# Kernel tuning notes

Hardware: AMD Instinct MI355X
Metric: run time of the kernel (lower is better)

Reference implementation:

```python
import jax, jax.numpy as jnp
import numpy as np

B, S, E, H, D, NE, R = 2, 2048, 2048, 16, 128, 8, 16
HALF = D // 2
THETA = 10000.0


def setup_inputs() -> dict:
    key = jax.random.key(0)
    ks = jax.random.split(key, 18)

    def w(k, shape, fan_in):
        return jax.random.normal(k, shape, jnp.float32) / np.float32(np.sqrt(fan_in))

    inp = {
        "x": jax.random.normal(ks[0], (B, S, E), jnp.float32),
        "expert_mask": jax.random.uniform(ks[1], (B, S, NE), dtype=jnp.float32),
    }
    for i, n in enumerate(("q", "k", "v")):
        inp["W" + n] = w(ks[2 + 3 * i], (H * D, E), E)
        inp["b" + n] = jnp.zeros((H * D,), jnp.float32)
        inp["A" + n] = w(ks[3 + 3 * i], (NE, R, E), E)
        inp["B" + n] = w(ks[4 + 3 * i], (H * D, NE, R), R)
    inp["Wo"] = w(ks[11], (E, H * D), H * D)
    inp["bo"] = jnp.zeros((E,), jnp.float32)
    inp["Ao"] = w(ks[12], (NE, R, H * D), H * D)
    inp["Bo"] = w(ks[13], (E, NE, R), R)
    return inp


def routed_linear(x, W, b, A, Bm, mask):
    """MaybeRoutedLinear: dense base + expert-routed low-rank path gated by mask [B,S,NE]."""
    y = jnp.einsum("bsi,oi->bso", x, W) + b
    h = jnp.einsum("bsi,eri->bser", x, A) * mask[..., None]  # [B,S,NE,R]
    return y + jnp.einsum("bser,oer->bso", h, Bm)


def apply_rope(t):
    """Llama-style rotary embedding. t: [B,S,H,D]."""
    inv_freq = 1.0 / (THETA ** (jnp.arange(0, D, 2, dtype=jnp.float32) / D))  # [D/2]
    freqs = jnp.arange(S, dtype=jnp.float32)[:, None] * inv_freq[None, :]  # [S,D/2]
    cos = jnp.concatenate([jnp.cos(freqs)] * 2, -1)[None, :, None, :]  # [1,S,1,D]
    sin = jnp.concatenate([jnp.sin(freqs)] * 2, -1)[None, :, None, :]
    rot = jnp.concatenate([-t[..., HALF:], t[..., :HALF]], -1)
    return t * cos + rot * sin


def reference(x, expert_mask, Wq, bq, Aq, Bq, Wk, bk, Ak, Bk, Wv, bv, Av, Bv, Wo, bo, Ao, Bo):
    q = routed_linear(x, Wq, bq, Aq, Bq, expert_mask).reshape(B, S, H, D)
    k = routed_linear(x, Wk, bk, Ak, Bk, expert_mask).reshape(B, S, H, D)
    v = routed_linear(x, Wv, bv, Av, Bv, expert_mask).reshape(B, S, H, D)
    q = apply_rope(q)
    k = apply_rope(k)
    scores = jnp.einsum("bqhd,bkhd->bhqk", q, k) / jnp.float32(np.sqrt(D))
    causal = jnp.tril(jnp.ones((S, S), dtype=bool))
    scores = jnp.where(causal[None, None], scores, jnp.finfo(scores.dtype).min)
    probs = jax.nn.softmax(scores, axis=-1)
    o = jnp.einsum("bhqk,bkhd->bqhd", probs, v).reshape(B, S, H * D)
    return routed_linear(o, Wo, bo, Ao, Bo, expert_mask)
```

## Files before the change

kernel.cpp:

```cpp
#include <hip/hip_runtime.h>


#define B_ 2
#define S_ 2048
#define E_ 2048
#define H_ 16
#define D_ 128
#define NE_ 8
#define R_ 16
#define HD_ 2048
#define M_ 4096
#define KL_ 128

typedef unsigned short u16;
typedef unsigned int u32;
typedef __attribute__((ext_vector_type(8))) short bf16x8;
typedef __attribute__((ext_vector_type(4))) float f32x4;

typedef const __attribute__((address_space(1))) void gvoid_t;
typedef __attribute__((address_space(3))) void svoid_t;

__device__ __forceinline__ float bf2f(u16 u) {
    union { u32 i; float f; } v; v.i = ((u32)u) << 16; return v.f;
}
__device__ __forceinline__ u16 f2bf(float f) {
    union { float f; u32 i; } v; v.f = f;
    u32 x = v.i;
    return (u16)((x + 0x7fffu + ((x >> 16) & 1u)) >> 16);
}
__device__ __forceinline__ float ldf(const void* p, size_t i, int f) {
    return f ? ((const float*)p)[i] : bf2f(((const u16*)p)[i]);
}
__device__ __forceinline__ float4 ld4(const void* p, size_t i, int f) {
    if (f) return *(const float4*)((const float*)p + i);
    ushort4 v = *(const ushort4*)((const u16*)p + i);
    return make_float4(bf2f(v.x), bf2f(v.y), bf2f(v.z), bf2f(v.w));
}

__global__ void k_detect(const void* __restrict__ x, int* __restrict__ flags) {
    __shared__ int votes[2];
    int tid = threadIdx.x;
    if (tid < 2) votes[tid] = 0;
    __syncthreads();
    const u32* p = (const u32*)x;
    int bad = 0, tot = 0;
    for (int i = tid; i < 4096; i += 64) {
        u32 lo = p[i] & 0xffffu;
        if (lo) {
            tot++;
            int e = (int)((lo >> 7) & 0xffu);
            if (e < 100 || e > 150) bad++;
        }
    }
    atomicAdd(&votes[0], bad);
    atomicAdd(&votes[1], tot);
    __syncthreads();
    if (tid == 0) flags[0] = (votes[1] > 0 && votes[0] * 10 > votes[1] * 3) ? 1 : 0;
}

__global__ void k_cvt(const void* __restrict__ src, u16* __restrict__ dst, int n,
                      const int* __restrict__ flags) {
    int fin = flags[0];
    int i = (blockIdx.x * 256 + threadIdx.x) * 4;
    if (i >= n) return;
    float4 v = ld4(src, i, fin);
    ushort4 o;
    o.x = f2bf(v.x); o.y = f2bf(v.y); o.z = f2bf(v.z); o.w = f2bf(v.w);
    *(ushort4*)(dst + i) = o;
}

__global__ void k_cvtf(const float* __restrict__ src, u16* __restrict__ dst, int n) {
    int i = (blockIdx.x * 256 + threadIdx.x) * 4;
    if (i >= n) return;
    float4 v = *(const float4*)(src + i);
    ushort4 o;
    o.x = f2bf(v.x); o.y = f2bf(v.y); o.z = f2bf(v.z); o.w = f2bf(v.w);
    *(ushort4*)(dst + i) = o;
}

__global__ void k_zero(float4* __restrict__ p, int n4) {
    int i = blockIdx.x * 256 + threadIdx.x;
    if (i < n4) p[i] = make_float4(0.f, 0.f, 0.f, 0.f);
}

#define NX_  8388608L
#define NA1_ 262144L
#define NW_  4194304L
__global__ void k_cvt_all(
    const void* __restrict__ x,
    const void* __restrict__ Aq, const void* __restrict__ Ak,
    const void* __restrict__ Av, const void* __restrict__ Ao,
    const void* __restrict__ Bq, const void* __restrict__ Bk,
    const void* __restrict__ Bv, const void* __restrict__ Bo,
    const void* __restrict__ Wq, const void* __restrict__ Wk,
    const void* __restrict__ Wv,
    u16* __restrict__ Xb, u16* __restrict__ Acat, u16* __restrict__ Bmcat,
    u16* __restrict__ Wcat,
    const int* __restrict__ flags) {
    int fin = flags[0];
    long i = (long)(blockIdx.x * 256 + threadIdx.x) * 4;
    const void* src; u16* dst; long off;
    if (i < NX_) { src = x; dst = Xb; off = i; }
    else if (i < NX_ + 4 * NA1_) {
        long j = i - NX_; int p = (int)(j >> 18); off = j & (NA1_ - 1);
        src = (p == 0) ? Aq : (p == 1) ? Ak : (p == 2) ? Av : Ao;
        dst = Acat + (long)p * NA1_;
    } else if (i < NX_ + 8 * NA1_) {
        long j = i - NX_ - 4 * NA1_; int p = (int)(j >> 18); off = j & (NA1_ - 1);
        src = (p == 0) ? Bq : (p == 1) ? Bk : (p == 2) ? Bv : Bo;
        dst = Bmcat + (long)p * NA1_;
    } else {
        long j = i - NX_ - 8 * NA1_; int p = (int)(j / NW_); off = j - (long)p * NW_;
        src = (p == 0) ? Wq : (p == 1) ? Wk : Wv;
        dst = Wcat + (long)p * NW_;
    }
    float4 v = ld4(src, off, fin);
    ushort4 o;
    o.x = f2bf(v.x); o.y = f2bf(v.y); o.z = f2bf(v.z); o.w = f2bf(v.w);
    *(ushort4*)(dst + off) = o;
}

#define BM_ 128
#define BN_ 128
#define BK_ 64

__global__ __launch_bounds__(256, 2) void k_gemm_sk(
    const u16* __restrict__ A, int lda,
    const u16* __restrict__ Bw, int ldb, int K,
    const void* __restrict__ mask,
    float* __restrict__ Cf, int ldc,
    const int* __restrict__ flags) {
    __shared__ __align__(16) u16 As[BM_ * BK_];
    __shared__ __align__(16) u16 Bs[BN_ * BK_];
    int fin = flags[0];
    int tid = threadIdx.x;
    int w = tid >> 6, lane = tid & 63;
    int l15 = lane & 15, quad = lane >> 4;
    int wm = w >> 1, wn = w & 1;
    int m0 = blockIdx.y * BM_, n0 = blockIdx.x * BN_;
    int lrow = lane >> 3;
    int lcol = (lane & 7) * 8;

    f32x4 acc[4][4];
#pragma unroll
    for (int mt = 0; mt < 4; mt++)
#pragma unroll
        for (int nt = 0; nt < 4; nt++)
#pragma unroll
            for (int r = 0; r < 4; r++) acc[mt][nt][r] = 0.f;

    int iters = (K / BK_) / gridDim.z;
    int it0 = blockIdx.z * iters;
    for (int it = it0; it < it0 + iters; it++) {
        int kb = it * BK_;
        __syncthreads();
#pragma unroll
        for (int i = 0; i < 4; i++) {
            int rowb = (w * 4 + i) * 8;
            int r = rowb + lrow;
            __builtin_amdgcn_global_load_lds(
                (gvoid_t*)(A + (size_t)(m0 + r) * lda + kb + lcol),
                (svoid_t*)(As + rowb * BK_), 16, 0, 0);
            __builtin_amdgcn_global_load_lds(
                (gvoid_t*)(Bw + (size_t)(n0 + r) * ldb + kb + lcol),
                (svoid_t*)(Bs + rowb * BK_), 16, 0, 0);
        }
        __syncthreads();
#pragma unroll
        for (int kk = 0; kk < 2; kk++) {
            int ko = kk * 32 + quad * 8;
            bf16x8 af[4], bf[4];
#pragma unroll
            for (int mt = 0; mt < 4; mt++)
                af[mt] = *(const bf16x8*)(As + (wm * 64 + mt * 16 + l15) * BK_ + ko);
#pragma unroll
            for (int nt = 0; nt < 4; nt++)
                bf[nt] = *(const bf16x8*)(Bs + (wn * 64 + nt * 16 + l15) * BK_ + ko);
#pragma unroll
            for (int mt = 0; mt < 4; mt++)
#pragma unroll
                for (int nt = 0; nt < 4; nt++)
                    acc[mt][nt] = __builtin_amdgcn_mfma_f32_16x16x32_bf16(
                        af[mt], bf[nt], acc[mt][nt], 0, 0, 0);
        }
    }

#pragma unroll
    for (int mt = 0; mt < 4; mt++) {
#pragma unroll
        for (int r = 0; r < 4; r++) {
            int m = m0 + wm * 64 + mt * 16 + quad * 4 + r;
#pragma unroll
            for (int nt = 0; nt < 4; nt++) {
                int n = n0 + wn * 64 + nt * 16 + l15;
                float v = acc[mt][nt][r] * ldf(mask, (size_t)m * NE_ + ((n & 127) >> 4), fin);
                atomicAdd(&Cf[(size_t)m * ldc + n], v);
            }
        }
    }
}

template <int BNt>
__global__ __launch_bounds__(512, 2) void k_gemm256(
    const u16* __restrict__ A, int lda,
    const u16* __restrict__ Bw, int ldb, int K1,
    const u16* __restrict__ A2, int lda2,
    const u16* __restrict__ B2, int K2,
    const void* __restrict__ bias0, const void* __restrict__ bias1,
    const void* __restrict__ bias2,
    void* __restrict__ C, int ldc, int store_mode,
    const int* __restrict__ flags) {
    constexpr int NTF = BNt / 64;
    __shared__ __align__(16) u16 As[2][256 * 32];
    __shared__ __align__(16) u16 Bs[2][BNt * 32];
    int fin = flags[0];
    int tid = threadIdx.x;
    int w = tid >> 6, lane = tid & 63;
    int l15 = lane & 15, quad = lane >> 4;
    int wm = w >> 2, wn = w & 3;

    int lin = blockIdx.y * gridDim.x + blockIdx.x;
    int cpx = (gridDim.x * gridDim.y) >> 3;
    int wg = (lin & 7) * cpx + (lin >> 3);
    int m0 = (wg / gridDim.x) * 256;
    int n0 = (wg % gridDim.x) * BNt;

    int p = (store_mode == 3) ? (n0 >> 11) : 0;
    const u16* A2p = A2 + p * 128;
    const u16* B2p = B2 + (long)p * NA1_;
    int nloc = (store_mode == 3) ? (n0 & 2047) : n0;

    int nk1 = K1 >> 5;
    int NT = nk1 + (K2 >> 5);

    f32x4 acc[8][NTF];
#pragma unroll
    for (int mt = 0; mt < 8; mt++)
#pragma unroll
        for (int nt = 0; nt < NTF; nt++)
#pragma unroll
            for (int r = 0; r < 4; r++) acc[mt][nt][r] = 0.f;

    auto stage = [&](int kt) {
        const u16 *pa, *pb; size_t sa, sb; int kb, nb;
        if (kt < nk1) { pa = A;   sa = lda;  pb = Bw;  sb = ldb; kb = kt * 32; nb = n0; }
        else          { pa = A2p; sa = lda2; pb = B2p; sb = K2;  kb = (kt - nk1) * 32; nb = nloc; }
        int buf = kt & 1;
#pragma unroll
        for (int j = 0; j < 2; j++) {
            int s = w * 2 + j;
            __builtin_amdgcn_global_load_lds(
                (gvoid_t*)(pa + (size_t)(m0 + s * 16 + l15) * sa + kb + quad * 8),
                (svoid_t*)(&As[buf][s * 512]), 16, 0, 0);
        }
        if constexpr (BNt == 256) {
#pragma unroll
            for (int j = 0; j < 2; j++) {
                int s = w * 2 + j;
                __builtin_amdgcn_global_load_lds(
                    (gvoid_t*)(pb + (size_t)(nb + s * 16 + l15) * sb + kb + quad * 8),
                    (svoid_t*)(&Bs[buf][s * 512]), 16, 0, 0);
            }
        } else {
            __builtin_amdgcn_global_load_lds(
                (gvoid_t*)(pb + (size_t)(nb + w * 16 + l15) * sb + kb + quad * 8),
                (svoid_t*)(&Bs[buf][w * 512]), 16, 0, 0);
        }
    };

    stage(0);
    for (int kt = 0; kt < NT; kt++) {
        int buf = kt & 1;
        if (kt + 1 < NT) {
            stage(kt + 1);
            if constexpr (BNt == 256) asm volatile("s_waitcnt vmcnt(4)" ::: "memory");
            else                      asm volatile("s_waitcnt vmcnt(3)" ::: "memory");
        } else {
            asm volatile("s_waitcnt vmcnt(0)" ::: "memory");
        }
        __builtin_amdgcn_s_barrier();
        __builtin_amdgcn_sched_barrier(0);

        bf16x8 af[8], bfr[NTF];
#pragma unroll
        for (int mt = 0; mt < 8; mt++)
            af[mt] = *(const bf16x8*)(&As[buf][(wm * 8 + mt) * 512 + lane * 8]);
#pragma unroll
        for (int nt = 0; nt < NTF; nt++)
            bfr[nt] = *(const bf16x8*)(&Bs[buf][(wn * NTF + nt) * 512 + lane * 8]);

        __builtin_amdgcn_s_setprio(1);
#pragma unroll
        for (int mt = 0; mt < 8; mt++)
#pragma unroll
            for (int nt = 0; nt < NTF; nt++)
                acc[mt][nt] = __builtin_amdgcn_mfma_f32_16x16x32_bf16(
                    af[mt], bfr[nt], acc[mt][nt], 0, 0, 0);
        __builtin_amdgcn_s_setprio(0);

        __builtin_amdgcn_s_barrier();
        __builtin_amdgcn_sched_barrier(0);
    }

    const void* bp = (store_mode == 3) ? (p == 0 ? bias0 : p == 1 ? bias1 : bias2)
                                       : bias0;
#pragma unroll
    for (int mt = 0; mt < 8; mt++) {
#pragma unroll
        for (int r = 0; r < 4; r++) {
            int m = m0 + wm * 128 + mt * 16 + quad * 4 + r;
#pragma unroll
            for (int nt = 0; nt < NTF; nt++) {
                int n = n0 + wn * (BNt / 4) + nt * 16 + l15;
                float v = acc[mt][nt][r];
                if (bp) v += ldf(bp, (size_t)(n & 2047), fin);
                if (store_mode == 3) {
                    ((u16*)C)[(size_t)p * 8388608 + (size_t)m * 2048 + (n & 2047)] = f2bf(v);
                } else {
                    if (fin) ((float*)C)[(size_t)m * ldc + n] = v;
                    else     ((u16*)C)[(size_t)m * ldc + n] = f2bf(v);
                }
            }
        }
    }
}

__global__ void k_rope2(u16* __restrict__ Q, u16* __restrict__ K) {
    const int n = M_ * HD_ / 2;
    int idx = blockIdx.x * 256 + threadIdx.x;
    u16* Y = (idx < n) ? Q : K;
    int id = (idx < n) ? idx : idx - n;
    int d2 = id & 63;
    int sh = id >> 6;
    int s = (sh >> 4) & (S_ - 1);
    float inv = powf(10000.f, -(float)d2 * (1.f / 64.f));
    float fr = (float)s * inv;
    float c, sn;
    sincosf(fr, &sn, &c);
    size_t base = ((size_t)sh) << 7;
    float t0 = bf2f(Y[base + d2]);
    float t1 = bf2f(Y[base + d2 + 64]);
    Y[base + d2]      = f2bf(t0 * c - t1 * sn);
    Y[base + d2 + 64] = f2bf(t1 * c + t0 * sn);
}

__global__ void k_transpose_v(const u16* __restrict__ Vb, u16* __restrict__ Vt) {
    __shared__ u16 t[32][33];
    int s0 = blockIdx.x * 32;
    int n0 = blockIdx.y * 32;
    int b  = blockIdx.z;
    int tx = threadIdx.x & 31, ty = threadIdx.x >> 5;
#pragma unroll
    for (int r = 0; r < 4; r++)
        t[ty + r * 8][tx] = Vb[((size_t)(b * S_ + s0 + ty + r * 8)) * HD_ + n0 + tx];
    __syncthreads();
#pragma unroll
    for (int r = 0; r < 4; r++)
        Vt[((size_t)(b * HD_ + n0 + ty + r * 8)) * S_ + s0 + tx] = t[tx][ty + r * 8];
}

#define KS_ST 136
#define VT_ST 72
#define SCALE_ 0.088388347648318447f

__global__ __launch_bounds__(256, 3) void k_flash6(
    const u16* __restrict__ Q, const u16* __restrict__ K,
    const u16* __restrict__ Vt, u16* __restrict__ O) {
    __shared__ __align__(16) u16 Ks[64 * KS_ST];
    __shared__ __align__(16) u16 Vs[128 * VT_ST];
    __shared__ __align__(16) u16 Ps[64 * VT_ST];
    int tid = threadIdx.x;
    int w = tid >> 6, lane = tid & 63;
    int l15 = lane & 15, quad = lane >> 4;
    int bh = blockIdx.y, b = bh >> 4, h = bh & 15;
    int t = 31 - blockIdx.x;
    int q0 = t * 64;

    int krow[4], kd8[4], vd[4], vkg[4];
#pragma unroll
    for (int it = 0; it < 4; it++) {
        int idx = it * 256 + tid;
        krow[it] = idx >> 4; kd8[it] = (idx & 15) * 8;
        vd[it] = idx >> 3;   vkg[it] = (idx & 7) * 8;
    }

    bf16x8 qf[4];
    size_t baseQ = ((size_t)(b * S_ + q0 + w * 16 + l15)) * HD_ + h * D_;
#pragma unroll
    for (int ks = 0; ks < 4; ks++)
        qf[ks] = *(const bf16x8*)(Q + baseQ + ks * 32 + quad * 8);

    f32x4 of[8];
#pragma unroll
    for (int nt = 0; nt < 8; nt++)
#pragma unroll
        for (int r = 0; r < 4; r++) of[nt][r] = 0.f;
    float mreg = -30000.f, lreg = 0.f;
    int qrow = q0 + w * 16 + l15;

    int nch = t + 1;

    bf16x8 kpre[4], vpre[4];
#pragma unroll
    for (int it = 0; it < 4; it++) {
        kpre[it] = *(const bf16x8*)(K + ((size_t)(b * S_ + krow[it])) * HD_ + h * D_ + kd8[it]);
        vpre[it] = *(const bf16x8*)(Vt + ((size_t)(bh * 128 + vd[it])) * S_ + vkg[it]);
    }

    for (int c = 0; c < nch; c++) {
        int k0 = c * 64;
        __syncthreads();
#pragma unroll
        for (int it = 0; it < 4; it++) {
            *(bf16x8*)(Ks + krow[it] * KS_ST + kd8[it]) = kpre[it];
            *(bf16x8*)(Vs + vd[it] * VT_ST + vkg[it]) = vpre[it];
        }
        __syncthreads();
        if (c + 1 < nch) {
            int k1 = k0 + 64;
#pragma unroll
            for (int it = 0; it < 4; it++) {
                kpre[it] = *(const bf16x8*)(K + ((size_t)(b * S_ + k1 + krow[it])) * HD_ + h * D_ + kd8[it]);
                vpre[it] = *(const bf16x8*)(Vt + ((size_t)(bh * 128 + vd[it])) * S_ + k1 + vkg[it]);
            }
        }

        f32x4 sf[4];
#pragma unroll
        for (int nt = 0; nt < 4; nt++)
#pragma unroll
            for (int r = 0; r < 4; r++) sf[nt][r] = 0.f;
#pragma unroll
        for (int ks = 0; ks < 4; ks++) {
            int koff = ks * 32 + quad * 8;
            bf16x8 qa = qf[ks];
#pragma unroll
            for (int nt = 0; nt < 4; nt++) {
                bf16x8 kb = *(const bf16x8*)(Ks + (nt * 16 + l15) * KS_ST + koff);
                sf[nt] = __builtin_amdgcn_mfma_f32_16x16x32_bf16(kb, qa, sf[nt], 0, 0, 0);
            }
        }

#pragma unroll
        for (int nt = 0; nt < 4; nt++) {
            int keyb = k0 + nt * 16 + quad * 4;
#pragma unroll
            for (int r = 0; r < 4; r++) {
                float sv = sf[nt][r] * SCALE_;
                sf[nt][r] = (keyb + r > qrow) ? -30000.f : sv;
            }
        }

        float t0 = fmaxf(fmaxf(sf[0][0], sf[0][1]), fmaxf(sf[0][2], sf[0][3]));
        float t1 = fmaxf(fmaxf(sf[1][0], sf[1][1]), fmaxf(sf[1][2], sf[1][3]));
        float t2 = fmaxf(fmaxf(sf[2][0], sf[2][1]), fmaxf(sf[2][2], sf[2][3]));
        float t3 = fmaxf(fmaxf(sf[3][0], sf[3][1]), fmaxf(sf[3][2], sf[3][3]));
        float cmax = fmaxf(fmaxf(t0, t1), fmaxf(t2, t3));
        cmax = fmaxf(cmax, __shfl_xor(cmax, 16, 64));
        cmax = fmaxf(cmax, __shfl_xor(cmax, 32, 64));
        float mnew = fmaxf(mreg, cmax);
        float a = __expf(mreg - mnew);
        mreg = mnew;
#pragma unroll
        for (int nt = 0; nt < 4; nt++)
#pragma unroll
            for (int r = 0; r < 4; r++)
                sf[nt][r] = __expf(sf[nt][r] - mnew);
        float s0 = (sf[0][0] + sf[0][1]) + (sf[0][2] + sf[0][3]);
        float s1 = (sf[1][0] + sf[1][1]) + (sf[1][2] + sf[1][3]);
        float s2 = (sf[2][0] + sf[2][1]) + (sf[2][2] + sf[2][3]);
        float s3 = (sf[3][0] + sf[3][1]) + (sf[3][2] + sf[3][3]);
        float psum = (s0 + s1) + (s2 + s3);
        psum += __shfl_xor(psum, 16, 64);
        psum += __shfl_xor(psum, 32, 64);
        lreg = lreg * a + psum;

        float al[4];
#pragma unroll
        for (int r = 0; r < 4; r++) al[r] = __shfl(a, quad * 4 + r, 16);

#pragma unroll
        for (int nt = 0; nt < 4; nt++)
#pragma unroll
            for (int r = 0; r < 4; r++)
                Ps[(w * 16 + l15) * VT_ST + nt * 16 + quad * 4 + r] = f2bf(sf[nt][r]);
#pragma unroll
        for (int nt = 0; nt < 8; nt++)
#pragma unroll
            for (int r = 0; r < 4; r++) of[nt][r] *= al[r];

#pragma unroll
        for (int ks2 = 0; ks2 < 2; ks2++) {
            int koff = ks2 * 32 + quad * 8;
            bf16x8 pa = *(const bf16x8*)(Ps + (w * 16 + l15) * VT_ST + koff);
#pragma unroll
            for (int nt = 0; nt < 8; nt++) {
                bf16x8 vb = *(const bf16x8*)(Vs + (nt * 16 + l15) * VT_ST + koff);
                of[nt] = __builtin_amdgcn_mfma_f32_16x16x32_bf16(pa, vb, of[nt], 0, 0, 0);
            }
        }
    }

    float linv = 1.f / lreg;
    float inv[4];
#pragma unroll
    for (int r = 0; r < 4; r++) inv[r] = __shfl(linv, quad * 4 + r, 16);
    int rowb = q0 + w * 16 + quad * 4;
#pragma unroll
    for (int r = 0; r < 4; r++) {
        size_t base = ((size_t)(b * S_ + rowb + r)) * HD_ + h * D_;
#pragma unroll
        for (int nt = 0; nt < 8; nt++)
            O[base + nt * 16 + l15] = f2bf(of[nt][r] * inv[r]);
    }
}

extern "C" void kernel_launch(void* const* d_in, const int* in_sizes, int n_in,
                              void* d_out, int out_size, void* d_ws, size_t ws_size,
                              hipStream_t stream) {
    const void* x    = d_in[0];
    const void* mask = d_in[1];
    const void* Wq = d_in[2];  const void* bq = d_in[3];
    const void* Aq = d_in[4];  const void* Bq = d_in[5];
    const void* Wk = d_in[6];  const void* bk = d_in[7];
    const void* Ak = d_in[8];  const void* Bk = d_in[9];
    const void* Wv = d_in[10]; const void* bv = d_in[11];
    const void* Av = d_in[12]; const void* Bv = d_in[13];
    const void* Wo = d_in[14]; const void* bo = d_in[15];
    const void* Ao = d_in[16]; const void* Bo = d_in[17];

    char* ws = (char*)d_ws;
    const long MB = 1 << 20;
    int* flags = (int*)ws;
    u16* Xb    = (u16*)(ws + 1  * MB);
    u16* Acat  = (u16*)(ws + 17 * MB);
    u16* Bmcat = (u16*)(ws + 19 * MB);
    u16* hg3   = (u16*)(ws + 21 * MB);
    u16* hgo   = (u16*)(ws + 24 * MB);
    u16* Qb    = (u16*)(ws + 25 * MB);
    u16* Kb    = (u16*)(ws + 41 * MB);
    u16* Vb    = (u16*)(ws + 57 * MB);
    u16* Vt    = (u16*)(ws + 73 * MB);
    u16* Wcat  = (u16*)(ws + 73 * MB);
    float* hg3f = (float*)Qb;
    float* hgof = (float*)Kb;
    u16* Wob   = Qb;
    u16* Ob    = Vb;

    k_detect<<<1, 64, 0, stream>>>(x, flags);
    k_zero<<<1536, 256, 0, stream>>>((float4*)hg3f, 393216);
    const long NCVT = NX_ + 8 * NA1_ + 3 * NW_;
    k_cvt_all<<<NCVT / 1024, 256, 0, stream>>>(
        x, Aq, Ak, Av, Ao, Bq, Bk, Bv, Bo, Wq, Wk, Wv,
        Xb, Acat, Bmcat, Wcat, flags);

    k_gemm_sk<<<dim3(3, M_ / BM_, 4), 256, 0, stream>>>(
        Xb, E_, Acat, E_, E_, mask, hg3f, 384, flags);
    k_cvtf<<<1536, 256, 0, stream>>>(hg3f, hg3, 1572864);

    k_gemm256<256><<<dim3(6144 / 256, M_ / 256), 512, 0, stream>>>(
        Xb, E_, Wcat, E_, E_, hg3, 384, Bmcat, KL_,
        bq, bk, bv, Qb, HD_, 3, flags);

    k_rope2<<<(M_ * HD_) / 256, 256, 0, stream>>>(Qb, Kb);
    k_transpose_v<<<dim3(S_ / 32, HD_ / 32, B_), 256, 0, stream>>>(Vb, Vt);

    k_flash6<<<dim3(32, 32), 256, 0, stream>>>(Qb, Kb, Vt, Ob);

    k_zero<<<512, 256, 0, stream>>>((float4*)hgof, 131072);
    k_cvt<<<NW_ / 1024, 256, 0, stream>>>(Wo, Wob, (int)NW_, flags);
    k_gemm_sk<<<dim3(1, M_ / BM_, 4), 256, 0, stream>>>(
        Ob, HD_, Acat + 3 * NA1_, E_, E_, mask, hgof, KL_, flags);
    k_cvtf<<<512, 256, 0, stream>>>(hgof, hgo, 524288);

    k_gemm256<128><<<dim3(HD_ / 128, M_ / 256), 512, 0, stream>>>(
        Ob, HD_, Wob, E_, E_, hgo, KL_, Bmcat + 3 * NA1_, KL_,
        bo, nullptr, nullptr, d_out, HD_, 2, flags);
}
```

Measured before the change: 797.5 us.

## Rework GEMM into 4-stage LDS pipeline with split-phase MFMA and prefetch

Replaces the double-buffered 256-row GEMM with a quad-buffered kernel that prefetches three K-tiles ahead. Each iteration is split into two MFMA phases, and the A and B prefetches are interleaved between them to overlap global-to-LDS loads with compute. The output GEMM switches from a 256x128 tile to a 128x256 tile. LDS use doubles and more barriers are added per iteration, which may limit occupancy at two blocks per CU.

After: 728.7 us. 8.6% less time.

```diff
diff --git a/kernel.cpp b/kernel.cpp
--- a/kernel.cpp
+++ b/kernel.cpp
@@ -200,8 +200,8 @@
     }
 }
 
-template <int BNt>
-__global__ __launch_bounds__(512, 2) void k_gemm256(
+template <int BMt>
+__global__ __launch_bounds__(512, 2) void k_gemm8p(
     const u16* __restrict__ A, int lda,
     const u16* __restrict__ Bw, int ldb, int K1,
     const u16* __restrict__ A2, int lda2,
@@ -210,9 +210,12 @@
     const void* __restrict__ bias2,
     void* __restrict__ C, int ldc, int store_mode,
     const int* __restrict__ flags) {
-    constexpr int NTF = BNt / 64;
-    __shared__ __align__(16) u16 As[2][256 * 32];
-    __shared__ __align__(16) u16 Bs[2][BNt * 32];
+    constexpr int MT  = BMt / 32;
+    constexpr int NSA = BMt / 16;
+    constexpr int LA  = BMt / 128;
+    constexpr int L   = LA + 2;
+    __shared__ __align__(16) u16 As[4][NSA * 512];
+    __shared__ __align__(16) u16 Bs[4][16 * 512];
     int fin = flags[0];
     int tid = threadIdx.x;
     int w = tid >> 6, lane = tid & 63;
@@ -222,8 +225,8 @@
     int lin = blockIdx.y * gridDim.x + blockIdx.x;
     int cpx = (gridDim.x * gridDim.y) >> 3;
     int wg = (lin & 7) * cpx + (lin >> 3);
-    int m0 = (wg / gridDim.x) * 256;
-    int n0 = (wg % gridDim.x) * BNt;
+    int m0 = (wg / gridDim.x) * BMt;
+    int n0 = (wg % gridDim.x) * 256;
 
     int p = (store_mode == 3) ? (n0 >> 11) : 0;
     const u16* A2p = A2 + p * 128;
@@ -233,85 +236,104 @@
     int nk1 = K1 >> 5;
     int NT = nk1 + (K2 >> 5);
 
-    f32x4 acc[8][NTF];
-#pragma unroll
-    for (int mt = 0; mt < 8; mt++)
-#pragma unroll
-        for (int nt = 0; nt < NTF; nt++)
+    f32x4 acc[MT][4];
+#pragma unroll
+    for (int mt = 0; mt < MT; mt++)
+#pragma unroll
+        for (int nt = 0; nt < 4; nt++)
 #pragma unroll
             for (int r = 0; r < 4; r++) acc[mt][nt][r] = 0.f;
 
-    auto stage = [&](int kt) {
-        const u16 *pa, *pb; size_t sa, sb; int kb, nb;
-        if (kt < nk1) { pa = A;   sa = lda;  pb = Bw;  sb = ldb; kb = kt * 32; nb = n0; }
-        else          { pa = A2p; sa = lda2; pb = B2p; sb = K2;  kb = (kt - nk1) * 32; nb = nloc; }
-        int buf = kt & 1;
+    auto stageA = [&](int kt) {
+        const u16* pa; size_t sa; int kb;
+        if (kt < nk1) { pa = A;   sa = (size_t)lda;  kb = kt * 32; }
+        else          { pa = A2p; sa = (size_t)lda2; kb = (kt - nk1) * 32; }
+        int buf = kt & 3;
+#pragma unroll
+        for (int j = 0; j < LA; j++) {
+            int rb = w * LA + j;
+            __builtin_amdgcn_global_load_lds(
+                (gvoid_t*)(pa + (size_t)(m0 + rb * 16 + l15) * sa + kb + quad * 8),
+                (svoid_t*)(&As[buf][rb * 512]), 16, 0, 0);
+        }
+    };
+    auto stageB = [&](int kt) {
+        const u16* pb; size_t sb; int kb, nb;
+        if (kt < nk1) { pb = Bw;  sb = (size_t)ldb; kb = kt * 32;          nb = n0; }
+        else          { pb = B2p; sb = (size_t)K2;  kb = (kt - nk1) * 32;  nb = nloc; }
+        int buf = kt & 3;
 #pragma unroll
         for (int j = 0; j < 2; j++) {
-            int s = w * 2 + j;
+            int rb = w * 2 + j;
             __builtin_amdgcn_global_load_lds(
-                (gvoid_t*)(pa + (size_t)(m0 + s * 16 + l15) * sa + kb + quad * 8),
-                (svoid_t*)(&As[buf][s * 512]), 16, 0, 0);
-        }
-        if constexpr (BNt == 256) {
-#pragma unroll
-            for (int j = 0; j < 2; j++) {
-                int s = w * 2 + j;
-                __builtin_amdgcn_global_load_lds(
-                    (gvoid_t*)(pb + (size_t)(nb + s * 16 + l15) * sb + kb + quad * 8),
-                    (svoid_t*)(&Bs[buf][s * 512]), 16, 0, 0);
-            }
-        } else {
-            __builtin_amdgcn_global_load_lds(
-                (gvoid_t*)(pb + (size_t)(nb + w * 16 + l15) * sb + kb + quad * 8),
-                (svoid_t*)(&Bs[buf][w * 512]), 16, 0, 0);
+                (gvoid_t*)(pb + (size_t)(nb + rb * 16 + l15) * sb + kb + quad * 8),
+                (svoid_t*)(&Bs[buf][rb * 512]), 16, 0, 0);
         }
     };
 
-    stage(0);
+    stageA(0); stageB(0);
+    stageA(1); stageB(1);
+    stageA(2); stageB(2);
+    if constexpr (L == 4) asm volatile("s_waitcnt vmcnt(8)" ::: "memory");
+    else                  asm volatile("s_waitcnt vmcnt(6)" ::: "memory");
+    __builtin_amdgcn_s_barrier();
+
     for (int kt = 0; kt < NT; kt++) {
-        int buf = kt & 1;
-        if (kt + 1 < NT) {
-            stage(kt + 1);
-            if constexpr (BNt == 256) asm volatile("s_waitcnt vmcnt(4)" ::: "memory");
-            else                      asm volatile("s_waitcnt vmcnt(3)" ::: "memory");
-        } else {
+        int buf = kt & 3;
+        bool pre = (kt + 3 < NT);
+
+        bf16x8 af[MT], bfr[4];
+#pragma unroll
+        for (int mt = 0; mt < MT; mt++)
+            af[mt] = *(const bf16x8*)(&As[buf][(wm * MT + mt) * 512 + lane * 8]);
+        bfr[0] = *(const bf16x8*)(&Bs[buf][(wn * 4 + 0) * 512 + lane * 8]);
+        bfr[1] = *(const bf16x8*)(&Bs[buf][(wn * 4 + 1) * 512 + lane * 8]);
+        if (pre) stageA(kt + 3);
+        __builtin_amdgcn_s_barrier();
+        asm volatile("s_waitcnt lgkmcnt(0)" ::: "memory");
+        __builtin_amdgcn_s_setprio(1);
+#pragma unroll
+        for (int mt = 0; mt < MT; mt++) {
+            acc[mt][0] = __builtin_amdgcn_mfma_f32_16x16x32_bf16(af[mt], bfr[0], acc[mt][0], 0, 0, 0);
+            acc[mt][1] = __builtin_amdgcn_mfma_f32_16x16x32_bf16(af[mt], bfr[1], acc[mt][1], 0, 0, 0);
+        }
+        __builtin_amdgcn_s_setprio(0);
+        __builtin_amdgcn_s_barrier();
+
+        bfr[2] = *(const bf16x8*)(&Bs[buf][(wn * 4 + 2) * 512 + lane * 8]);
+        bfr[3] = *(const bf16x8*)(&Bs[buf][(wn * 4 + 3) * 512 + lane * 8]);
+        if (pre) stageB(kt + 3);
+        __builtin_amdgcn_s_barrier();
+        asm volatile("s_waitcnt lgkmcnt(0)" ::: "memory");
+        __builtin_amdgcn_s_setprio(1);
+#pragma unroll
+        for (int mt = 0; mt < MT; mt++) {
+            acc[mt][2] = __builtin_amdgcn_mfma_f32_16x16x32_bf16(af[mt], bfr[2], acc[mt][2], 0, 0, 0);
+            acc[mt][3] = __builtin_amdgcn_mfma_f32_16x16x32_bf16(af[mt], bfr[3], acc[mt][3], 0, 0, 0);
+        }
+        __builtin_amdgcn_s_setprio(0);
+        if (kt + 4 <= NT) {
+            if constexpr (L == 4) asm volatile("s_waitcnt vmcnt(8)" ::: "memory");
+            else                  asm volatile("s_waitcnt vmcnt(6)" ::: "memory");
+        } else if (kt + 3 == NT) {
+            if constexpr (L == 4) asm volatile("s_waitcnt vmcnt(4)" ::: "memory");
+            else                  asm volatile("s_waitcnt vmcnt(3)" ::: "memory");
+        } else if (kt + 2 == NT) {
             asm volatile("s_waitcnt vmcnt(0)" ::: "memory");
         }
         __builtin_amdgcn_s_barrier();
-        __builtin_amdgcn_sched_barrier(0);
-
-        bf16x8 af[8], bfr[NTF];
-#pragma unroll
-        for (int mt = 0; mt < 8; mt++)
-            af[mt] = *(const bf16x8*)(&As[buf][(wm * 8 + mt) * 512 + lane * 8]);
-#pragma unroll
-        for (int nt = 0; nt < NTF; nt++)
-            bfr[nt] = *(const bf16x8*)(&Bs[buf][(wn * NTF + nt) * 512 + lane * 8]);
-
-        __builtin_amdgcn_s_setprio(1);
-#pragma unroll
-        for (int mt = 0; mt < 8; mt++)
-#pragma unroll
-            for (int nt = 0; nt < NTF; nt++)
-                acc[mt][nt] = __builtin_amdgcn_mfma_f32_16x16x32_bf16(
-                    af[mt], bfr[nt], acc[mt][nt], 0, 0, 0);
-        __builtin_amdgcn_s_setprio(0);
-
-        __builtin_amdgcn_s_barrier();
-        __builtin_amdgcn_sched_barrier(0);
     }
 
     const void* bp = (store_mode == 3) ? (p == 0 ? bias0 : p == 1 ? bias1 : bias2)
                                        : bias0;
 #pragma unroll
-    for (int mt = 0; mt < 8; mt++) {
+    for (int mt = 0; mt < MT; mt++) {
 #pragma unroll
         for (int r = 0; r < 4; r++) {
-            int m = m0 + wm * 128 + mt * 16 + quad * 4 + r;
-#pragma unroll
-            for (int nt = 0; nt < NTF; nt++) {
-                int n = n0 + wn * (BNt / 4) + nt * 16 + l15;
+            int m = m0 + wm * (BMt / 2) + mt * 16 + quad * 4 + r;
+#pragma unroll
+            for (int nt = 0; nt < 4; nt++) {
+                int n = n0 + wn * 64 + nt * 16 + l15;
                 float v = acc[mt][nt][r];
                 if (bp) v += ldf(bp, (size_t)(n & 2047), fin);
                 if (store_mode == 3) {
@@ -558,7 +580,7 @@
         Xb, E_, Acat, E_, E_, mask, hg3f, 384, flags);
     k_cvtf<<<1536, 256, 0, stream>>>(hg3f, hg3, 1572864);
 
-    k_gemm256<256><<<dim3(6144 / 256, M_ / 256), 512, 0, stream>>>(
+    k_gemm8p<256><<<dim3(6144 / 256, M_ / 256), 512, 0, stream>>>(
         Xb, E_, Wcat, E_, E_, hg3, 384, Bmcat, KL_,
         bq, bk, bv, Qb, HD_, 3, flags);
 
@@ -573,7 +595,7 @@
         Ob, HD_, Acat + 3 * NA1_, E_, E_, mask, hgof, KL_, flags);
     k_cvtf<<<512, 256, 0, stream>>>(hgof, hgo, 524288);
 
-    k_gemm256<128><<<dim3(HD_ / 128, M_ / 256), 512, 0, stream>>>(
+    k_gemm8p<128><<<dim3(HD_ / 256, M_ / 128), 512, 0, stream>>>(
         Ob, HD_, Wob, E_, E_, hgo, KL_, Bmcat + 3 * NA1_, KL_,
         bo, nullptr, nullptr, d_out, HD_, 2, flags);
 }
```

## Restructure bf16 GEMM into 8-phase ping-pong schedule with K=64 tiles

Applied to the files above, without the earlier changes.

The 256-row GEMM kernel now stages K in 64-wide chunks instead of 32 and splits each iteration into four MFMA phases. Each phase interleaves LDS fragment reads and half-tile global-to-LDS prefetches (A for the next step, B two steps ahead) with barriers and priority toggling. The goal is to hide global load and LDS read latency behind matrix-core work and to halve loop and barrier overhead per K. In exchange the synchronisation is far more intricate, with hand-tuned vmcnt values and doubled LDS use that could lower occupancy or introduce races.

Measured after the change: 734.6 us. 1.09x faster.

```diff
diff --git a/kernel.cpp b/kernel.cpp
--- a/kernel.cpp
+++ b/kernel.cpp
@@ -201,7 +201,7 @@
 }
 
 template <int BNt>
-__global__ __launch_bounds__(512, 2) void k_gemm256(
+__global__ __launch_bounds__(512, 2) void k_gemm8p(
     const u16* __restrict__ A, int lda,
     const u16* __restrict__ Bw, int ldb, int K1,
     const u16* __restrict__ A2, int lda2,
@@ -211,8 +211,9 @@
     void* __restrict__ C, int ldc, int store_mode,
     const int* __restrict__ flags) {
     constexpr int NTF = BNt / 64;
-    __shared__ __align__(16) u16 As[2][256 * 32];
-    __shared__ __align__(16) u16 Bs[2][BNt * 32];
+    constexpr int NT0 = NTF / 2;
+    __shared__ __align__(16) u16 As[2 * 256 * 64];
+    __shared__ __align__(16) u16 Bs[2 * BNt * 64];
     int fin = flags[0];
     int tid = threadIdx.x;
     int w = tid >> 6, lane = tid & 63;
@@ -230,8 +231,8 @@
     const u16* B2p = B2 + (long)p * NA1_;
     int nloc = (store_mode == 3) ? (n0 & 2047) : n0;
 
-    int nk1 = K1 >> 5;
-    int NT = nk1 + (K2 >> 5);
+    int nk1 = K1 >> 6;
+    int NT = nk1 + (K2 >> 6);
 
     f32x4 acc[8][NTF];
 #pragma unroll
@@ -241,65 +242,138 @@
 #pragma unroll
             for (int r = 0; r < 4; r++) acc[mt][nt][r] = 0.f;
 
-    auto stage = [&](int kt) {
-        const u16 *pa, *pb; size_t sa, sb; int kb, nb;
-        if (kt < nk1) { pa = A;   sa = lda;  pb = Bw;  sb = ldb; kb = kt * 32; nb = n0; }
-        else          { pa = A2p; sa = lda2; pb = B2p; sb = K2;  kb = (kt - nk1) * 32; nb = nloc; }
-        int buf = kt & 1;
+    auto stageA = [&](int s, int h) {
+        const u16* pa; size_t sa; int kc;
+        if (s < nk1) { pa = A;   sa = (size_t)lda;  kc = s * 64; }
+        else         { pa = A2p; sa = (size_t)lda2; kc = (s - nk1) * 64; }
+        int base = ((s & 1) * 32 + h * 16) * 512;
 #pragma unroll
         for (int j = 0; j < 2; j++) {
-            int s = w * 2 + j;
+            int g = w * 2 + j;
             __builtin_amdgcn_global_load_lds(
-                (gvoid_t*)(pa + (size_t)(m0 + s * 16 + l15) * sa + kb + quad * 8),
-                (svoid_t*)(&As[buf][s * 512]), 16, 0, 0);
-        }
-        if constexpr (BNt == 256) {
-#pragma unroll
-            for (int j = 0; j < 2; j++) {
-                int s = w * 2 + j;
-                __builtin_amdgcn_global_load_lds(
-                    (gvoid_t*)(pb + (size_t)(nb + s * 16 + l15) * sb + kb + quad * 8),
-                    (svoid_t*)(&Bs[buf][s * 512]), 16, 0, 0);
-            }
-        } else {
+                (gvoid_t*)(pa + (size_t)(m0 + h * 128 + (g >> 1) * 16 + l15) * sa
+                           + kc + (g & 1) * 32 + quad * 8),
+                (svoid_t*)(As + base + g * 512), 16, 0, 0);
+        }
+    };
+    auto stageB = [&](int s, int h) {
+        const u16* pb; size_t sb; int kc, nb;
+        if (s < nk1) { pb = Bw;  sb = (size_t)ldb; kc = s * 64;          nb = n0; }
+        else         { pb = B2p; sb = (size_t)K2;  kc = (s - nk1) * 64;  nb = nloc; }
+        int base = (BNt == 256) ? ((s & 1) * 32 + h * 16) * 512
+                                : ((s & 1) * 16) * 512;
+#pragma unroll
+        for (int j = 0; j < 2; j++) {
+            int g = w * 2 + j;
             __builtin_amdgcn_global_load_lds(
-                (gvoid_t*)(pb + (size_t)(nb + w * 16 + l15) * sb + kb + quad * 8),
-                (svoid_t*)(&Bs[buf][w * 512]), 16, 0, 0);
+                (gvoid_t*)(pb + (size_t)(nb + h * 128 + (g >> 1) * 16 + l15) * sb
+                           + kc + (g & 1) * 32 + quad * 8),
+                (svoid_t*)(Bs + base + g * 512), 16, 0, 0);
         }
     };
 
-    stage(0);
-    for (int kt = 0; kt < NT; kt++) {
-        int buf = kt & 1;
-        if (kt + 1 < NT) {
-            stage(kt + 1);
+    stageA(0, 0); stageA(0, 1);
+    stageB(0, 0); if constexpr (BNt == 256) stageB(0, 1);
+    if (NT > 1) { stageB(1, 0); if constexpr (BNt == 256) stageB(1, 1); }
+    if (NT > 1) {
+        if constexpr (BNt == 256) asm volatile("s_waitcnt vmcnt(4)" ::: "memory");
+        else                      asm volatile("s_waitcnt vmcnt(2)" ::: "memory");
+    } else {
+        asm volatile("s_waitcnt vmcnt(0)" ::: "memory");
+    }
+    __builtin_amdgcn_s_barrier();
+
+    for (int t = 0; t < NT; t++) {
+        int dA = (t & 1) * 32 + wm * 16;
+        int dB = (BNt == 256) ? ((t & 1) * 32 + (wn >> 1) * 16) : ((t & 1) * 16);
+        bf16x8 af[4][2], bf[NTF][2];
+
+#pragma unroll
+        for (int mt = 0; mt < 4; mt++)
+#pragma unroll
+            for (int kh = 0; kh < 2; kh++)
+                af[mt][kh] = *(const bf16x8*)(As + (dA + mt * 2 + kh) * 512 + lane * 8);
+#pragma unroll
+        for (int nt = 0; nt < NT0; nt++) {
+            int nsub = (BNt == 256) ? ((wn & 1) * 4 + nt) : (wn * 2 + nt);
+#pragma unroll
+            for (int kh = 0; kh < 2; kh++)
+                bf[nt][kh] = *(const bf16x8*)(Bs + (dB + nsub * 2 + kh) * 512 + lane * 8);
+        }
+        if (t + 1 < NT) stageA(t + 1, 0);
+        __builtin_amdgcn_s_barrier();
+        asm volatile("s_waitcnt lgkmcnt(0)" ::: "memory");
+        __builtin_amdgcn_sched_barrier(0);
+        __builtin_amdgcn_s_setprio(1);
+#pragma unroll
+        for (int mt = 0; mt < 4; mt++)
+#pragma unroll
+            for (int nt = 0; nt < NT0; nt++) {
+                acc[mt][nt] = __builtin_amdgcn_mfma_f32_16x16x32_bf16(af[mt][0], bf[nt][0], acc[mt][nt], 0, 0, 0);
+                acc[mt][nt] = __builtin_amdgcn_mfma_f32_16x16x32_bf16(af[mt][1], bf[nt][1], acc[mt][nt], 0, 0, 0);
+            }
+        __builtin_amdgcn_s_setprio(0);
+        __builtin_amdgcn_s_barrier();
+
+#pragma unroll
+        for (int nt = NT0; nt < NTF; nt++) {
+            int nsub = (BNt == 256) ? ((wn & 1) * 4 + nt) : (wn * 2 + nt);
+#pragma unroll
+            for (int kh = 0; kh < 2; kh++)
+                bf[nt][kh] = *(const bf16x8*)(Bs + (dB + nsub * 2 + kh) * 512 + lane * 8);
+        }
+        if (t + 1 < NT) stageA(t + 1, 1);
+        __builtin_amdgcn_s_barrier();
+        asm volatile("s_waitcnt lgkmcnt(0)" ::: "memory");
+        __builtin_amdgcn_sched_barrier(0);
+        __builtin_amdgcn_s_setprio(1);
+#pragma unroll
+        for (int mt = 0; mt < 4; mt++)
+#pragma unroll
+            for (int nt = NT0; nt < NTF; nt++) {
+                acc[mt][nt] = __builtin_amdgcn_mfma_f32_16x16x32_bf16(af[mt][0], bf[nt][0], acc[mt][nt], 0, 0, 0);
+                acc[mt][nt] = __builtin_amdgcn_mfma_f32_16x16x32_bf16(af[mt][1], bf[nt][1], acc[mt][nt], 0, 0, 0);
+            }
+        __builtin_amdgcn_s_setprio(0);
+        __builtin_amdgcn_s_barrier();
+
+#pragma unroll
+        for (int mt = 0; mt < 4; mt++)
+#pragma unroll
+            for (int kh = 0; kh < 2; kh++)
+                af[mt][kh] = *(const bf16x8*)(As + (dA + (4 + mt) * 2 + kh) * 512 + lane * 8);
+        if (t + 2 < NT) stageB(t + 2, 0);
+        __builtin_amdgcn_s_barrier();
+        asm volatile("s_waitcnt lgkmcnt(0)" ::: "memory");
+        __builtin_amdgcn_sched_barrier(0);
+        __builtin_amdgcn_s_setprio(1);
+#pragma unroll
+        for (int mt = 0; mt < 4; mt++)
+#pragma unroll
+            for (int nt = NT0; nt < NTF; nt++) {
+                acc[4 + mt][nt] = __builtin_amdgcn_mfma_f32_16x16x32_bf16(af[mt][0], bf[nt][0], acc[4 + mt][nt], 0, 0, 0);
+                acc[4 + mt][nt] = __builtin_amdgcn_mfma_f32_16x16x32_bf16(af[mt][1], bf[nt][1], acc[4 + mt][nt], 0, 0, 0);
+            }
+        __builtin_amdgcn_s_setprio(0);
+        __builtin_amdgcn_s_barrier();
+
+        if constexpr (BNt == 256) { if (t + 2 < NT) stageB(t + 2, 1); }
+        __builtin_amdgcn_s_setprio(1);
+#pragma unroll
+        for (int mt = 0; mt < 4; mt++)
+#pragma unroll
+            for (int nt = 0; nt < NT0; nt++) {
+                acc[4 + mt][nt] = __builtin_amdgcn_mfma_f32_16x16x32_bf16(af[mt][0], bf[nt][0], acc[4 + mt][nt], 0, 0, 0);
+                acc[4 + mt][nt] = __builtin_amdgcn_mfma_f32_16x16x32_bf16(af[mt][1], bf[nt][1], acc[4 + mt][nt], 0, 0, 0);
+            }
+        __builtin_amdgcn_s_setprio(0);
+        if (t + 2 < NT) {
             if constexpr (BNt == 256) asm volatile("s_waitcnt vmcnt(4)" ::: "memory");
-            else                      asm volatile("s_waitcnt vmcnt(3)" ::: "memory");
-        } else {
+            else                      asm volatile("s_waitcnt vmcnt(2)" ::: "memory");
+        } else if (t + 1 < NT) {
             asm volatile("s_waitcnt vmcnt(0)" ::: "memory");
         }
         __builtin_amdgcn_s_barrier();
-        __builtin_amdgcn_sched_barrier(0);
-
-        bf16x8 af[8], bfr[NTF];
-#pragma unroll
-        for (int mt = 0; mt < 8; mt++)
-            af[mt] = *(const bf16x8*)(&As[buf][(wm * 8 + mt) * 512 + lane * 8]);
-#pragma unroll
-        for (int nt = 0; nt < NTF; nt++)
-            bfr[nt] = *(const bf16x8*)(&Bs[buf][(wn * NTF + nt) * 512 + lane * 8]);
-
-        __builtin_amdgcn_s_setprio(1);
-#pragma unroll
-        for (int mt = 0; mt < 8; mt++)
-#pragma unroll
-            for (int nt = 0; nt < NTF; nt++)
-                acc[mt][nt] = __builtin_amdgcn_mfma_f32_16x16x32_bf16(
-                    af[mt], bfr[nt], acc[mt][nt], 0, 0, 0);
-        __builtin_amdgcn_s_setprio(0);
-
-        __builtin_amdgcn_s_barrier();
-        __builtin_amdgcn_sched_barrier(0);
     }
 
     const void* bp = (store_mode == 3) ? (p == 0 ? bias0 : p == 1 ? bias1 : bias2)
@@ -558,7 +632,7 @@
         Xb, E_, Acat, E_, E_, mask, hg3f, 384, flags);
     k_cvtf<<<1536, 256, 0, stream>>>(hg3f, hg3, 1572864);
 
-    k_gemm256<256><<<dim3(6144 / 256, M_ / 256), 512, 0, stream>>>(
+    k_gemm8p<256><<<dim3(6144 / 256, M_ / 256), 512, 0, stream>>>(
         Xb, E_, Wcat, E_, E_, hg3, 384, Bmcat, KL_,
         bq, bk, bv, Qb, HD_, 3, flags);
 
@@ -573,7 +647,7 @@
         Ob, HD_, Acat + 3 * NA1_, E_, E_, mask, hgof, KL_, flags);
     k_cvtf<<<512, 256, 0, stream>>>(hgof, hgo, 524288);
 
-    k_gemm256<128><<<dim3(HD_ / 128, M_ / 256), 512, 0, stream>>>(
+    k_gemm8p<128><<<dim3(HD_ / 128, M_ / 256), 512, 0, stream>>>(
         Ob, HD_, Wob, E_, E_, hgo, KL_, Bmcat + 3 * NA1_, KL_,
         bo, nullptr, nullptr, d_out, HD_, 2, flags);
 }
```
